# Performance work log

Hardware: AMD Instinct MI355X
Metric: run time of the kernel (lower is better)

The kernel has to match this reference:

```python
import jax, jax.numpy as jnp
import numpy as np
import math

EPS = 1e-8
NUM_FREQS = 64
NUM_BINS = 128
NUM_QUERIES = 32768
HEAD_DIM = NUM_FREQS * 2


def setup_inputs() -> dict:
    key = jax.random.key(0)
    k1, k2, k3, k4, k5 = jax.random.split(key, 5)
    init_value = math.log(math.e - 1.0)
    return {
        "Q": jax.random.normal(k1, (NUM_QUERIES, HEAD_DIM), dtype=jnp.float32),
        "rotated_probes": jax.random.normal(k2, (NUM_BINS, HEAD_DIM), dtype=jnp.float32),
        # faithful init is full(init_value); add small noise so grads are non-degenerate
        "q_weights_raw": init_value + 0.1 * jax.random.normal(k3, (NUM_BINS, NUM_FREQS), dtype=jnp.float32),
        "q_magnitude_weights": 0.1 * jax.random.normal(k4, (NUM_BINS, NUM_FREQS), dtype=jnp.float32),
        "q_bias": 0.1 * jax.random.normal(k5, (NUM_BINS,), dtype=jnp.float32),
    }


def reference(Q, rotated_probes, q_weights_raw, q_magnitude_weights, q_bias):
    F = NUM_FREQS
    # L2-normalize queries (use_l2_norm=True)
    Qn = Q / (jnp.linalg.norm(Q, axis=-1, keepdims=True) + EPS)  # (q, d)
    Q_real, Q_imag = Qn[:, :F], Qn[:, F:]                        # (q, f)
    P_real, P_imag = rotated_probes[:, :F], rotated_probes[:, F:]  # (b, f)
    # per-frequency complex error and distance: (q, b, f)
    error_real = P_real[None, :, :] - Q_real[:, None, :]
    error_imag = P_imag[None, :, :] - Q_imag[:, None, :]
    distance = jnp.sqrt(error_real ** 2 + error_imag ** 2 + EPS)
    # per-frequency magnitude of normalized Q: (q, f)
    Q_magnitude = jnp.sqrt(Q_real ** 2 + Q_imag ** 2 + EPS)
    # negative weights via softplus
    effective_weights = -jax.nn.softplus(q_weights_raw)          # (b, f)
    distance_term = jnp.einsum('qbf,bf->qb', distance, effective_weights)
    magnitude_term = Q_magnitude @ q_magnitude_weights.T          # (q, b)
    scores = distance_term + magnitude_term + q_bias[None, :]
    return scores
```

## Files before the change

### kernel.cpp

```cpp
#include <hip/hip_runtime.h>
#include <math.h>

#define NUM_FREQS   64
#define NUM_BINS    128
#define NUM_QUERIES 32768
#define HEAD_DIM    128
#define EPS         1e-8f
#define NQB         16
#define SRP         (NQB + 1)

__global__ void prep_probe(const float* __restrict__ rp,
                           const float* __restrict__ wraw,
                           const float* __restrict__ mw,
                           float4* __restrict__ probeA,
                           float*  __restrict__ probeM) {
    int idx = blockIdx.x * 256 + threadIdx.x;
    if (idx >= NUM_FREQS * NUM_BINS) return;
    int f = idx >> 7;
    int b = idx & 127;
    float pr = rp[b * HEAD_DIM + f];
    float pi = rp[b * HEAD_DIM + NUM_FREQS + f];
    float w  = wraw[b * NUM_FREQS + f];
    float sp = fmaxf(w, 0.0f) + log1pf(expf(-fabsf(w)));
    probeA[idx] = make_float4(-2.0f * pr, -2.0f * pi,
                              fmaf(pr, pr, pi * pi), -sp);
    probeM[idx] = mw[b * NUM_FREQS + f];
}

__global__ __launch_bounds__(256, 4) void main_kernel(
        const float4* __restrict__ probeA,
        const float*  __restrict__ probeM,
        const float*  __restrict__ Q,
        const float*  __restrict__ bias,
        float*        __restrict__ out) {
    __shared__ float2 sri[NUM_FREQS + 1][SRP];
    __shared__ float  sqm[NUM_FREQS + 1][NQB];

    const int tid   = threadIdx.x;
    const int qbase = blockIdx.x * NQB;

    {
        const float4* Qb = reinterpret_cast<const float4*>(Q + (size_t)qbase * HEAD_DIM);
        float4 v1 = Qb[tid];
        float4 v2 = Qb[tid + 256];
        const int c  = tid & 31;
        const int r1 = tid >> 5;
        const int r2 = r1 + 8;

        float s1 = fmaf(v1.x, v1.x, fmaf(v1.y, v1.y, fmaf(v1.z, v1.z, v1.w * v1.w)));
        float s2 = fmaf(v2.x, v2.x, fmaf(v2.y, v2.y, fmaf(v2.z, v2.z, v2.w * v2.w)));
        #pragma unroll
        for (int off = 1; off < 32; off <<= 1) {
            s1 += __shfl_xor(s1, off);
            s2 += __shfl_xor(s2, off);
        }
        float inv1 = 1.0f / (__builtin_amdgcn_sqrtf(s1) + EPS);
        float inv2 = 1.0f / (__builtin_amdgcn_sqrtf(s2) + EPS);

        const float a1[4] = { v1.x, v1.y, v1.z, v1.w };
        const float a2[4] = { v2.x, v2.y, v2.z, v2.w };
        if (c < 16) {
            #pragma unroll
            for (int k = 0; k < 4; k++) {
                int row = 4 * c + k;
                sri[row][r1].x = a1[k] * inv1;
                sri[row][r2].x = a2[k] * inv2;
            }
        } else {
            #pragma unroll
            for (int k = 0; k < 4; k++) {
                int row = 4 * (c - 16) + k;
                sri[row][r1].y = a1[k] * inv1;
                sri[row][r2].y = a2[k] * inv2;
            }
        }
    }
    __syncthreads();
    #pragma unroll
    for (int i = 0; i < 4; i++) {
        int e = i * 256 + tid;
        int f = e >> 4, j = e & 15;
        float2 ri = sri[f][j];
        sqm[f][j] = __builtin_amdgcn_sqrtf(fmaf(ri.x, ri.x, fmaf(ri.y, ri.y, EPS)));
    }
    __syncthreads();

    const int lane = tid & 63;
    const int wave = tid >> 6;
    const int jb   = wave * 4;

    float b0 = bias[lane];
    float b1 = bias[64 + lane];

    float acc0[4], acc1[4];
    #pragma unroll
    for (int p = 0; p < 4; p++) { acc0[p] = 0.0f; acc1[p] = 0.0f; }

    const float4* pA = probeA + lane;
    const float*  pM = probeM + lane;

#define CSTEP(P0_, P1_, w0_, w1_, qa_, qb_, qc_, qd_, qm_)                   \
    {                                                                        \
        const float qrv[4] = { qa_.x, qb_.x, qc_.x, qd_.x };                 \
        const float qiv[4] = { qa_.y, qb_.y, qc_.y, qd_.y };                 \
        const float qmv[4] = { qm_.x, qm_.y, qm_.z, qm_.w };                 \
        _Pragma("unroll")                                                    \
        for (int p = 0; p < 4; p++) {                                        \
            float qr = qrv[p], qi = qiv[p], qm = qmv[p];                     \
            float a0 = fmaf(qm, qm, P0_.z);                                  \
            a0 = fmaf(P0_.x, qr, a0);                                        \
            a0 = fmaf(P0_.y, qi, a0);                                        \
            float d0 = __builtin_amdgcn_sqrtf(a0);                           \
            acc0[p] = fmaf(d0, P0_.w, fmaf(qm, w0_, acc0[p]));               \
            float a1 = fmaf(qm, qm, P1_.z);                                  \
            a1 = fmaf(P1_.x, qr, a1);                                        \
            a1 = fmaf(P1_.y, qi, a1);                                        \
            float d1 = __builtin_amdgcn_sqrtf(a1);                           \
            acc1[p] = fmaf(d1, P1_.w, fmaf(qm, w1_, acc1[p]));               \
        }                                                                    \
    }

    float4 A_P0 = pA[0], A_P1 = pA[64];
    float  A_w0 = pM[0], A_w1 = pM[64];
    float2 A_q0 = sri[0][jb],     A_q1 = sri[0][jb + 1];
    float2 A_q2 = sri[0][jb + 2], A_q3 = sri[0][jb + 3];
    float4 A_qm = *reinterpret_cast<const float4*>(&sqm[0][jb]);
    pA += NUM_BINS; pM += NUM_BINS;

    #pragma unroll 2
    for (int g = 0; g < NUM_FREQS / 2; ++g) {
        const int f1 = 2 * g + 1;
        float4 B_P0 = pA[0], B_P1 = pA[64];
        float  B_w0 = pM[0], B_w1 = pM[64];
        float2 B_q0 = sri[f1][jb],     B_q1 = sri[f1][jb + 1];
        float2 B_q2 = sri[f1][jb + 2], B_q3 = sri[f1][jb + 3];
        float4 B_qm = *reinterpret_cast<const float4*>(&sqm[f1][jb]);
        pA += NUM_BINS; pM += NUM_BINS;
        __builtin_amdgcn_sched_barrier(0);
        CSTEP(A_P0, A_P1, A_w0, A_w1, A_q0, A_q1, A_q2, A_q3, A_qm);

        A_P0 = pA[0]; A_P1 = pA[64];
        A_w0 = pM[0]; A_w1 = pM[64];
        A_q0 = sri[f1 + 1][jb];     A_q1 = sri[f1 + 1][jb + 1];
        A_q2 = sri[f1 + 1][jb + 2]; A_q3 = sri[f1 + 1][jb + 3];
        A_qm = *reinterpret_cast<const float4*>(&sqm[f1 + 1][jb]);
        pA += NUM_BINS; pM += NUM_BINS;
        __builtin_amdgcn_sched_barrier(0);
        CSTEP(B_P0, B_P1, B_w0, B_w1, B_q0, B_q1, B_q2, B_q3, B_qm);
    }
#undef CSTEP

    #pragma unroll
    for (int p = 0; p < 4; p++) {
        size_t row = (size_t)(qbase + jb + p) * NUM_BINS;
        out[row + lane]      = acc0[p] + b0;
        out[row + 64 + lane] = acc1[p] + b1;
    }
}

__global__ void fallback_kernel(const float* __restrict__ Q,
                                const float* __restrict__ rp,
                                const float* __restrict__ wraw,
                                const float* __restrict__ mw,
                                const float* __restrict__ bias,
                                float* __restrict__ out) {
    __shared__ float qn[HEAD_DIM];
    __shared__ float qmag[NUM_FREQS];
    __shared__ float red[NUM_BINS];
    const int t = threadIdx.x;
    const int q = blockIdx.x;

    float v = Q[(size_t)q * HEAD_DIM + t];
    red[t] = v * v;
    __syncthreads();
    for (int s = 64; s > 0; s >>= 1) {
        if (t < s) red[t] += red[t + s];
        __syncthreads();
    }
    float inv = 1.0f / (__builtin_amdgcn_sqrtf(red[0]) + EPS);
    qn[t] = v * inv;
    __syncthreads();
    if (t < NUM_FREQS) {
        float a = qn[t], c = qn[t + NUM_FREQS];
        qmag[t] = __builtin_amdgcn_sqrtf(fmaf(a, a, fmaf(c, c, EPS)));
    }
    __syncthreads();

    const int b = t;
    float acc = 0.0f;
    for (int f = 0; f < NUM_FREQS; f++) {
        float pr = rp[(size_t)b * HEAD_DIM + f];
        float pi = rp[(size_t)b * HEAD_DIM + NUM_FREQS + f];
        float w  = wraw[(size_t)b * NUM_FREQS + f];
        float ew = -(fmaxf(w, 0.0f) + log1pf(expf(-fabsf(w))));
        float er = pr - qn[f];
        float ei = pi - qn[f + NUM_FREQS];
        float d  = __builtin_amdgcn_sqrtf(fmaf(er, er, fmaf(ei, ei, EPS)));
        acc = fmaf(d, ew, fmaf(qmag[f], mw[(size_t)b * NUM_FREQS + f], acc));
    }
    out[(size_t)q * NUM_BINS + b] = acc + bias[b];
}

extern "C" void kernel_launch(void* const* d_in, const int* in_sizes, int n_in,
                              void* d_out, int out_size, void* d_ws, size_t ws_size,
                              hipStream_t stream) {
    const float* Q    = (const float*)d_in[0];
    const float* rp   = (const float*)d_in[1];
    const float* wraw = (const float*)d_in[2];
    const float* mw   = (const float*)d_in[3];
    const float* bias = (const float*)d_in[4];
    float* out = (float*)d_out;

    const size_t pABytes = (size_t)NUM_FREQS * NUM_BINS * sizeof(float4);
    const size_t pMBytes = (size_t)NUM_FREQS * NUM_BINS * sizeof(float);
    const size_t need    = pABytes + pMBytes + 8192;

    if (ws_size >= need) {
        float4* probeA = (float4*)d_ws;
        float*  probeM = (float*)((char*)d_ws + pABytes);

        hipLaunchKernelGGL(prep_probe, dim3(32), dim3(256), 0, stream,
                           rp, wraw, mw, probeA, probeM);
        hipLaunchKernelGGL(main_kernel, dim3(NUM_QUERIES / NQB), dim3(256), 0,
                           stream, probeA, probeM, Q, bias, out);
    } else {
        hipLaunchKernelGGL(fallback_kernel, dim3(NUM_QUERIES), dim3(NUM_BINS), 0,
                           stream, Q, rp, wraw, mw, bias, out);
    }
}
```

Baseline: 64.25 us.

## Interleave probe data and repack LDS query tile for wide vector loads

Measured after the change: 68.95 us. 7.3% more time.

```diff
diff --git a/kernel.cpp b/kernel.cpp
--- a/kernel.cpp
+++ b/kernel.cpp
@@ -7,48 +7,54 @@
 #define HEAD_DIM    128
 #define EPS         1e-8f
 #define NQB         16
-#define SRP         (NQB + 1)
+#define QROW        52
 
 __global__ void prep_probe(const float* __restrict__ rp,
                            const float* __restrict__ wraw,
                            const float* __restrict__ mw,
-                           float4* __restrict__ probeA,
-                           float*  __restrict__ probeM) {
+                           float4* __restrict__ probeP,
+                           float2* __restrict__ probeW) {
     int idx = blockIdx.x * 256 + threadIdx.x;
     if (idx >= NUM_FREQS * NUM_BINS) return;
     int f = idx >> 7;
     int b = idx & 127;
+    int l = b & 63, half = b >> 6;
     float pr = rp[b * HEAD_DIM + f];
     float pi = rp[b * HEAD_DIM + NUM_FREQS + f];
     float w  = wraw[b * NUM_FREQS + f];
     float sp = fmaxf(w, 0.0f) + log1pf(expf(-fabsf(w)));
-    probeA[idx] = make_float4(-2.0f * pr, -2.0f * pi,
-                              fmaf(pr, pr, pi * pi), -sp);
-    probeM[idx] = mw[b * NUM_FREQS + f];
+    probeP[(f * 64 + l) * 2 + half] =
+        make_float4(-2.0f * pr, -2.0f * pi, fmaf(pr, pr, pi * pi), -sp);
+    reinterpret_cast<float*>(&probeW[f * 64 + l])[half] = mw[b * NUM_FREQS + f];
 }
 
 __global__ __launch_bounds__(256, 4) void main_kernel(
-        const float4* __restrict__ probeA,
-        const float*  __restrict__ probeM,
+        const float4* __restrict__ probeP,
+        const float2* __restrict__ probeW,
         const float*  __restrict__ Q,
         const float*  __restrict__ bias,
         float*        __restrict__ out) {
-    __shared__ float2 sri[NUM_FREQS + 1][SRP];
-    __shared__ float  sqm[NUM_FREQS + 1][NQB];
+    __shared__ __align__(16) float srq[(NUM_FREQS + 1) * QROW];
 
     const int tid   = threadIdx.x;
     const int qbase = blockIdx.x * NQB;
 
     {
-        const float4* Qb = reinterpret_cast<const float4*>(Q + (size_t)qbase * HEAD_DIM);
-        float4 v1 = Qb[tid];
-        float4 v2 = Qb[tid + 256];
         const int c  = tid & 31;
         const int r1 = tid >> 5;
         const int r2 = r1 + 8;
-
-        float s1 = fmaf(v1.x, v1.x, fmaf(v1.y, v1.y, fmaf(v1.z, v1.z, v1.w * v1.w)));
-        float s2 = fmaf(v2.x, v2.x, fmaf(v2.y, v2.y, fmaf(v2.z, v2.z, v2.w * v2.w)));
+        const float* Q1 = Q + (size_t)(qbase + r1) * HEAD_DIM + c;
+        const float* Q2 = Q + (size_t)(qbase + r2) * HEAD_DIM + c;
+        float a1[4], a2[4];
+        #pragma unroll
+        for (int k = 0; k < 4; k++) {
+            a1[k] = Q1[32 * k];
+            a2[k] = Q2[32 * k];
+        }
+        float s1 = fmaf(a1[0], a1[0], fmaf(a1[1], a1[1],
+                   fmaf(a1[2], a1[2], a1[3] * a1[3])));
+        float s2 = fmaf(a2[0], a2[0], fmaf(a2[1], a2[1],
+                   fmaf(a2[2], a2[2], a2[3] * a2[3])));
         #pragma unroll
         for (int off = 1; off < 32; off <<= 1) {
             s1 += __shfl_xor(s1, off);
@@ -57,31 +63,20 @@
         float inv1 = 1.0f / (__builtin_amdgcn_sqrtf(s1) + EPS);
         float inv2 = 1.0f / (__builtin_amdgcn_sqrtf(s2) + EPS);
 
-        const float a1[4] = { v1.x, v1.y, v1.z, v1.w };
-        const float a2[4] = { v2.x, v2.y, v2.z, v2.w };
-        if (c < 16) {
-            #pragma unroll
-            for (int k = 0; k < 4; k++) {
-                int row = 4 * c + k;
-                sri[row][r1].x = a1[k] * inv1;
-                sri[row][r2].x = a2[k] * inv2;
-            }
-        } else {
-            #pragma unroll
-            for (int k = 0; k < 4; k++) {
-                int row = 4 * (c - 16) + k;
-                sri[row][r1].y = a1[k] * inv1;
-                sri[row][r2].y = a2[k] * inv2;
-            }
+        #define PUT_CELL(ff, jj_, qr_, qi_)                                   \
+        {                                                                     \
+            int w_ = (jj_) >> 2, j_ = (jj_) & 3;                              \
+            float* p_ = srq + (ff) * QROW + w_ * 12;                          \
+            *reinterpret_cast<float2*>(p_ + ((j_ >> 1) << 2) + ((j_ & 1) << 1)) \
+                = make_float2(qr_, qi_);                                      \
+            p_[8 + j_] = __builtin_amdgcn_sqrtf(                              \
+                fmaf(qr_, qr_, fmaf(qi_, qi_, EPS)));                         \
         }
-    }
-    __syncthreads();
-    #pragma unroll
-    for (int i = 0; i < 4; i++) {
-        int e = i * 256 + tid;
-        int f = e >> 4, j = e & 15;
-        float2 ri = sri[f][j];
-        sqm[f][j] = __builtin_amdgcn_sqrtf(fmaf(ri.x, ri.x, fmaf(ri.y, ri.y, EPS)));
+        PUT_CELL(c,      r1, a1[0] * inv1, a1[2] * inv1);
+        PUT_CELL(c + 32, r1, a1[1] * inv1, a1[3] * inv1);
+        PUT_CELL(c,      r2, a2[0] * inv2, a2[2] * inv2);
+        PUT_CELL(c + 32, r2, a2[1] * inv2, a2[3] * inv2);
+        #undef PUT_CELL
     }
     __syncthreads();
 
@@ -96,13 +91,14 @@
     #pragma unroll
     for (int p = 0; p < 4; p++) { acc0[p] = 0.0f; acc1[p] = 0.0f; }
 
-    const float4* pA = probeA + lane;
-    const float*  pM = probeM + lane;
-
-#define CSTEP(P0_, P1_, w0_, w1_, qa_, qb_, qc_, qd_, qm_)                   \
+    const float*  sqp = srq + wave * 12;
+    const float4* pP  = probeP + lane * 2;
+    const float2* pW  = probeW + lane;
+
+#define CSTEP(P0_, P1_, ww_, r01_, r23_, qm_)                                \
     {                                                                        \
-        const float qrv[4] = { qa_.x, qb_.x, qc_.x, qd_.x };                 \
-        const float qiv[4] = { qa_.y, qb_.y, qc_.y, qd_.y };                 \
+        const float qrv[4] = { r01_.x, r01_.z, r23_.x, r23_.z };             \
+        const float qiv[4] = { r01_.y, r01_.w, r23_.y, r23_.w };             \
         const float qmv[4] = { qm_.x, qm_.y, qm_.z, qm_.w };                 \
         _Pragma("unroll")                                                    \
         for (int p = 0; p < 4; p++) {                                        \
@@ -111,42 +107,41 @@
             a0 = fmaf(P0_.x, qr, a0);                                        \
             a0 = fmaf(P0_.y, qi, a0);                                        \
             float d0 = __builtin_amdgcn_sqrtf(a0);                           \
-            acc0[p] = fmaf(d0, P0_.w, fmaf(qm, w0_, acc0[p]));               \
+            acc0[p] = fmaf(d0, P0_.w, fmaf(qm, ww_.x, acc0[p]));             \
             float a1 = fmaf(qm, qm, P1_.z);                                  \
             a1 = fmaf(P1_.x, qr, a1);                                        \
             a1 = fmaf(P1_.y, qi, a1);                                        \
             float d1 = __builtin_amdgcn_sqrtf(a1);                           \
-            acc1[p] = fmaf(d1, P1_.w, fmaf(qm, w1_, acc1[p]));               \
+            acc1[p] = fmaf(d1, P1_.w, fmaf(qm, ww_.y, acc1[p]));             \
         }                                                                    \
     }
 
-    float4 A_P0 = pA[0], A_P1 = pA[64];
-    float  A_w0 = pM[0], A_w1 = pM[64];
-    float2 A_q0 = sri[0][jb],     A_q1 = sri[0][jb + 1];
-    float2 A_q2 = sri[0][jb + 2], A_q3 = sri[0][jb + 3];
-    float4 A_qm = *reinterpret_cast<const float4*>(&sqm[0][jb]);
-    pA += NUM_BINS; pM += NUM_BINS;
+    float4 A_P0 = pP[0], A_P1 = pP[1];
+    float2 A_ww = pW[0];
+    float4 A_r01 = *reinterpret_cast<const float4*>(sqp);
+    float4 A_r23 = *reinterpret_cast<const float4*>(sqp + 4);
+    float4 A_qm  = *reinterpret_cast<const float4*>(sqp + 8);
+    sqp += QROW; pP += 128; pW += 64;
 
     #pragma unroll 2
     for (int g = 0; g < NUM_FREQS / 2; ++g) {
-        const int f1 = 2 * g + 1;
-        float4 B_P0 = pA[0], B_P1 = pA[64];
-        float  B_w0 = pM[0], B_w1 = pM[64];
-        float2 B_q0 = sri[f1][jb],     B_q1 = sri[f1][jb + 1];
-        float2 B_q2 = sri[f1][jb + 2], B_q3 = sri[f1][jb + 3];
-        float4 B_qm = *reinterpret_cast<const float4*>(&sqm[f1][jb]);
-        pA += NUM_BINS; pM += NUM_BINS;
+        float4 B_P0 = pP[0], B_P1 = pP[1];
+        float2 B_ww = pW[0];
+        float4 B_r01 = *reinterpret_cast<const float4*>(sqp);
+        float4 B_r23 = *reinterpret_cast<const float4*>(sqp + 4);
+        float4 B_qm  = *reinterpret_cast<const float4*>(sqp + 8);
+        sqp += QROW; pP += 128; pW += 64;
         __builtin_amdgcn_sched_barrier(0);
-        CSTEP(A_P0, A_P1, A_w0, A_w1, A_q0, A_q1, A_q2, A_q3, A_qm);
-
-        A_P0 = pA[0]; A_P1 = pA[64];
-        A_w0 = pM[0]; A_w1 = pM[64];
-        A_q0 = sri[f1 + 1][jb];     A_q1 = sri[f1 + 1][jb + 1];
-        A_q2 = sri[f1 + 1][jb + 2]; A_q3 = sri[f1 + 1][jb + 3];
-        A_qm = *reinterpret_cast<const float4*>(&sqm[f1 + 1][jb]);
-        pA += NUM_BINS; pM += NUM_BINS;
+        CSTEP(A_P0, A_P1, A_ww, A_r01, A_r23, A_qm);
+
+        A_P0 = pP[0]; A_P1 = pP[1];
+        A_ww = pW[0];
+        A_r01 = *reinterpret_cast<const float4*>(sqp);
+        A_r23 = *reinterpret_cast<const float4*>(sqp + 4);
+        A_qm  = *reinterpret_cast<const float4*>(sqp + 8);
+        sqp += QROW; pP += 128; pW += 64;
         __builtin_amdgcn_sched_barrier(0);
-        CSTEP(B_P0, B_P1, B_w0, B_w1, B_q0, B_q1, B_q2, B_q3, B_qm);
+        CSTEP(B_P0, B_P1, B_ww, B_r01, B_r23, B_qm);
     }
 #undef CSTEP
 
@@ -211,18 +206,18 @@
     const float* bias = (const float*)d_in[4];
     float* out = (float*)d_out;
 
-    const size_t pABytes = (size_t)NUM_FREQS * NUM_BINS * sizeof(float4);
-    const size_t pMBytes = (size_t)NUM_FREQS * NUM_BINS * sizeof(float);
-    const size_t need    = pABytes + pMBytes + 8192;
+    const size_t pPBytes = (size_t)NUM_FREQS * 64 * 2 * sizeof(float4);
+    const size_t pWBytes = (size_t)NUM_FREQS * 64 * sizeof(float2);
+    const size_t need    = pPBytes + pWBytes + 8192;
 
     if (ws_size >= need) {
-        float4* probeA = (float4*)d_ws;
-        float*  probeM = (float*)((char*)d_ws + pABytes);
+        float4* probeP = (float4*)d_ws;
+        float2* probeW = (float2*)((char*)d_ws + pPBytes);
 
         hipLaunchKernelGGL(prep_probe, dim3(32), dim3(256), 0, stream,
-                           rp, wraw, mw, probeA, probeM);
+                           rp, wraw, mw, probeP, probeW);
         hipLaunchKernelGGL(main_kernel, dim3(NUM_QUERIES / NQB), dim3(256), 0,
-                           stream, probeA, probeM, Q, bias, out);
+                           stream, probeP, probeW, Q, bias, out);
     } else {
         hipLaunchKernelGGL(fallback_kernel, dim3(NUM_QUERIES), dim3(NUM_BINS), 0,
                            stream, Q, rp, wraw, mw, bias, out);
```
